# Performance work log

Measured on AMD Instinct MI355X. Metric: run time of the kernel, lower is better.

Reference implementation:

```python
import jax, jax.numpy as jnp
import numpy as np

D_MODEL = 1024
N_HEAD = 16
D_K = D_MODEL // N_HEAD


def setup_inputs() -> dict:
    key = jax.random.key(0)
    ks = jax.random.split(key, 11)
    B, S = 2, 2048
    scale = 1.0 / np.sqrt(D_MODEL)
    inp = {
        "q": jax.random.normal(ks[0], (B, S, D_MODEL), jnp.float32),
        "k": jax.random.normal(ks[1], (B, S, D_MODEL), jnp.float32),
        "v": jax.random.normal(ks[2], (B, S, D_MODEL), jnp.float32),
        "Wq": jax.random.normal(ks[3], (D_MODEL, D_MODEL), jnp.float32) * scale,
        "bq": jnp.zeros((D_MODEL,), jnp.float32),
        "Wk": jax.random.normal(ks[4], (D_MODEL, D_MODEL), jnp.float32) * scale,
        "bk": jnp.zeros((D_MODEL,), jnp.float32),
        "Wv": jax.random.normal(ks[5], (D_MODEL, D_MODEL), jnp.float32) * scale,
        "bv": jnp.zeros((D_MODEL,), jnp.float32),
        "Wo": jax.random.normal(ks[6], (D_MODEL, D_MODEL), jnp.float32) * scale,
        "bo": jnp.zeros((D_MODEL,), jnp.float32),
    }
    return inp


def reference(q, k, v, Wq, bq, Wk, bk, Wv, bv, Wo, bo):
    B, S, _ = q.shape
    # QKV projections, split heads: [B, H, S, d_k]
    def proj(x, W, b):
        y = x @ W + b  # [B, S, D]
        return y.reshape(B, -1, N_HEAD, D_K).transpose(0, 2, 1, 3)

    qh = proj(q, Wq, bq)
    kh = proj(k, Wk, bk)
    vh = proj(v, Wv, bv)

    # sigmoid attention (no row normalization)
    scores = jnp.einsum("bhsd,bhtd->bhst", qh, kh) / jnp.sqrt(jnp.float32(D_K))
    attn = jax.nn.sigmoid(scores)  # [B, H, S, S]
    ctx = jnp.einsum("bhst,bhtd->bhsd", attn, vh)

    # merge heads and output projection
    ctx = ctx.transpose(0, 2, 1, 3).reshape(B, S, D_MODEL)
    return ctx @ Wo + bo
```

## Files before the change

kernel.cpp:

```cpp
#include <hip/hip_runtime.h>
#include <stdint.h>

typedef _Float16 f16;
typedef _Float16 f16x4 __attribute__((ext_vector_type(4)));
typedef _Float16 f16x8 __attribute__((ext_vector_type(8)));
typedef float f32x4 __attribute__((ext_vector_type(4)));

#define D_MODEL 1024
#define N_HEAD 16
#define BATCH 2
#define SEQ 2048
#define MTOT 4096
#define NQKV 3072

__device__ __forceinline__ void llds16(const void* g, void* l) {
  __builtin_amdgcn_global_load_lds(
      (const __attribute__((address_space(1))) unsigned int*)g,
      (__attribute__((address_space(3))) unsigned int*)l, 16, 0, 0);
}

__device__ __forceinline__ float fast_rcp(float x) {
#if __has_builtin(__builtin_amdgcn_rcpf)
  return __builtin_amdgcn_rcpf(x);
#else
  return 1.0f / x;
#endif
}

__global__ void k_cvt(const float* __restrict__ src, f16* __restrict__ dst, int n) {
  int i = (blockIdx.x * blockDim.x + threadIdx.x) * 4;
  if (i < n) {
    const float4 v = *(const float4*)(src + i);
    f16x4 o;
    o.x = (f16)v.x; o.y = (f16)v.y; o.z = (f16)v.z; o.w = (f16)v.w;
    *(f16x4*)(dst + i) = o;
  }
}

__global__ void k_tw(const float* __restrict__ Wq, const float* __restrict__ Wk,
                     const float* __restrict__ Wv, const float* __restrict__ Wo,
                     f16* __restrict__ WqkvT, f16* __restrict__ WoT) {
  __shared__ float t[32][33];
  const int z = blockIdx.z;
  const float* W = (z == 0) ? Wq : (z == 1) ? Wk : (z == 2) ? Wv : Wo;
  f16* dst = (z < 3) ? (WqkvT + (size_t)z * 1024 * 1024) : WoT;
  const int bx = blockIdx.x * 32, by = blockIdx.y * 32;
  const int tx = threadIdx.x, ty = threadIdx.y;
#pragma unroll
  for (int i = 0; i < 32; i += 8)
    t[ty + i][tx] = W[(size_t)(by + ty + i) * 1024 + bx + tx];
  __syncthreads();
#pragma unroll
  for (int i = 0; i < 32; i += 8)
    dst[(size_t)(bx + ty + i) * 1024 + by + tx] = (f16)t[tx][ty + i];
}

template <int Nd, bool OUTF32>
__global__ __launch_bounds__(512, 4) void k_gemm(const f16* __restrict__ A0,
                                                 const f16* __restrict__ A1,
                                                 const f16* __restrict__ A2,
                                                 const f16* __restrict__ BT,
                                                 const float* __restrict__ b0,
                                                 const float* __restrict__ b1,
                                                 const float* __restrict__ b2,
                                                 void* __restrict__ Cout) {
  constexpr int Kd = 1024;
  constexpr int NBX = Nd / 128;
  constexpr int NWG = (MTOT / 128) * NBX;
  __shared__ __align__(16) f16 As[2][8192];
  __shared__ __align__(16) f16 Bs[2][8192];
  int id = blockIdx.x;
  id = (id & 7) * (NWG / 8) + (id >> 3);
  const int n0 = (id % NBX) * 128, m0 = (id / NBX) * 128;
  const f16* A = (Nd == 1024) ? A0 : (n0 < 1024 ? A0 : n0 < 2048 ? A1 : A2);
  const int tid = threadIdx.x, w = tid >> 6, ln = tid & 63;
  const int wm = w >> 2, wn = w & 3;
  f32x4 acc[4][2] = {};

  auto stage = [&](int buf, int kt) {
    const int k0 = kt * 64;
#pragma unroll
    for (int i = 0; i < 2; ++i) {
      const int c = w * 2 + i;
      const int r = c * 8 + (ln >> 3);
      const int g = ln & 7;
      const int ko = k0 + ((g ^ (r & 7)) * 8);
      llds16(A + (size_t)(m0 + r) * Kd + ko, &As[buf][c * 512]);
      llds16(BT + (size_t)(n0 + r) * Kd + ko, &Bs[buf][c * 512]);
    }
  };
  stage(0, 0);
  __syncthreads();
  int cur = 0;
  for (int kt = 0; kt < Kd / 64; ++kt) {
    if (kt < Kd / 64 - 1) stage(cur ^ 1, kt + 1);
#pragma unroll
    for (int kk = 0; kk < 2; ++kk) {
      f16x8 af[4], bf[2];
#pragma unroll
      for (int mi = 0; mi < 4; ++mi) {
        const int r = wm * 64 + mi * 16 + (ln & 15);
        const int g = kk * 4 + (ln >> 4);
        af[mi] = *(const f16x8*)(&As[cur][r * 64 + ((g ^ (r & 7)) * 8)]);
      }
#pragma unroll
      for (int nf = 0; nf < 2; ++nf) {
        const int r = wn * 32 + nf * 16 + (ln & 15);
        const int g = kk * 4 + (ln >> 4);
        bf[nf] = *(const f16x8*)(&Bs[cur][r * 64 + ((g ^ (r & 7)) * 8)]);
      }
#pragma unroll
      for (int mi = 0; mi < 4; ++mi)
#pragma unroll
        for (int nf = 0; nf < 2; ++nf)
          acc[mi][nf] = __builtin_amdgcn_mfma_f32_16x16x32_f16(af[mi], bf[nf], acc[mi][nf], 0, 0, 0);
    }
    __syncthreads();
    cur ^= 1;
  }
  const float* bb = (Nd == 1024) ? b0 : (n0 < 1024 ? b0 : n0 < 2048 ? b1 : b2);
  const int nb = n0 & 1023;
#pragma unroll
  for (int mi = 0; mi < 4; ++mi)
#pragma unroll
    for (int nf = 0; nf < 2; ++nf)
#pragma unroll
      for (int r = 0; r < 4; ++r) {
        const int row = m0 + wm * 64 + mi * 16 + (ln >> 4) * 4 + r;
        const int cl = wn * 32 + nf * 16 + (ln & 15);
        const float val = acc[mi][nf][r] + bb[nb + cl];
        if (OUTF32)
          ((float*)Cout)[(size_t)row * Nd + n0 + cl] = val;
        else
          ((f16*)Cout)[(size_t)row * Nd + n0 + cl] = (f16)val;
      }
}

__global__ void k_tv(const f16* __restrict__ QKV, f16* __restrict__ Vt) {
  const int sb = blockIdx.x, h = blockIdx.y, b = blockIdx.z;
  const int t = threadIdx.x;
  const int d = t & 63, si = (t >> 6) * 16;
  const int s0 = sb * 64 + si;
  const f16* src = QKV + ((size_t)b * SEQ + s0) * NQKV + 2048 + h * 64 + d;
  f16x8 v0, v1;
#pragma unroll
  for (int j = 0; j < 8; ++j) v0[j] = src[(size_t)j * NQKV];
#pragma unroll
  for (int j = 0; j < 8; ++j) v1[j] = src[(size_t)(j + 8) * NQKV];
  f16* dst = Vt + ((size_t)(b * N_HEAD + h) * 64 + d) * SEQ + s0;
  *(f16x8*)dst = v0;
  *(f16x8*)(dst + 8) = v1;
}

__global__ __launch_bounds__(256, 4) void k_attn(const f16* __restrict__ QKV,
                                                 const f16* __restrict__ Vt,
                                                 f16* __restrict__ ctx) {
  __shared__ __align__(16) f16 Ks[2][4096];
  __shared__ __align__(16) f16 Vs[2][4096];
  __shared__ __align__(16) f16 Pl[4][1024];
  int id = blockIdx.x;
  id = (id & 7) * 128 + (id >> 3);
  const int qt = id & 31, h = (id >> 5) & 15, b = id >> 9;
  const int tid = threadIdx.x, w = tid >> 6, ln = tid & 63;
  const int s0 = qt * 64;
  const f16* Qb = QKV + ((size_t)b * SEQ) * NQKV + h * 64;
  const f16* Kb = QKV + ((size_t)b * SEQ) * NQKV + 1024 + h * 64;
  const f16* Vtb = Vt + (size_t)(b * N_HEAD + h) * 64 * SEQ;
  const int q = ln & 15;
  f16x8 aq[2];
  {
    const int qrow = s0 + w * 16 + q;
#pragma unroll
    for (int kk = 0; kk < 2; ++kk)
      aq[kk] = *(const f16x8*)(Qb + (size_t)qrow * NQKV + kk * 32 + (ln >> 4) * 8);
  }
  f32x4 oacc[4] = {};
  auto stage = [&](int buf, int kt) {
    const int kv0 = kt * 64;
#pragma unroll
    for (int i = 0; i < 2; ++i) {
      const int c = w * 2 + i;
      const int r = c * 8 + (ln >> 3);
      const int g = ln & 7;
      llds16(Kb + (size_t)(kv0 + r) * NQKV + ((g ^ (r & 7)) * 8), &Ks[buf][c * 512]);
      llds16(Vtb + (size_t)r * SEQ + kv0 + ((g ^ (r & 7)) * 8), &Vs[buf][c * 512]);
    }
  };
  stage(0, 0);
  __syncthreads();
  int cur = 0;
  for (int kt = 0; kt < SEQ / 64; ++kt) {
    if (kt < SEQ / 64 - 1) stage(cur ^ 1, kt + 1);
    f32x4 sacc[4] = {};
#pragma unroll
    for (int kk = 0; kk < 2; ++kk) {
      f16x8 ak[4];
#pragma unroll
      for (int nt = 0; nt < 4; ++nt) {
        const int kv = nt * 16 + (ln & 15);
        const int g = kk * 4 + (ln >> 4);
        ak[nt] = *(const f16x8*)(&Ks[cur][kv * 64 + ((g ^ (kv & 7)) * 8)]);
      }
#pragma unroll
      for (int nt = 0; nt < 4; ++nt)
        sacc[nt] = __builtin_amdgcn_mfma_f32_16x16x32_f16(ak[nt], aq[kk], sacc[nt], 0, 0, 0);
    }
#pragma unroll
    for (int nt = 0; nt < 4; ++nt) {
      f16x4 pk;
#pragma unroll
      for (int r = 0; r < 4; ++r) {
        const float e = __expf(sacc[nt][r] * -0.125f);
        pk[r] = (f16)fast_rcp(1.0f + e);
      }
      const int gw = nt * 4 + (ln >> 4);
      *(f16x4*)(&Pl[w][q * 64 + ((gw ^ (2 * (q & 7))) * 4)]) = pk;
    }
#pragma unroll
    for (int kk = 0; kk < 2; ++kk) {
      const int gr = kk * 8 + (ln >> 4) * 2;
      const f16x8 ap = *(const f16x8*)(&Pl[w][q * 64 + ((gr ^ (2 * (q & 7))) * 4)]);
      f16x8 bv[4];
#pragma unroll
      for (int nt = 0; nt < 4; ++nt) {
        const int d = nt * 16 + (ln & 15);
        const int g = kk * 4 + (ln >> 4);
        bv[nt] = *(const f16x8*)(&Vs[cur][d * 64 + ((g ^ (d & 7)) * 8)]);
      }
#pragma unroll
      for (int nt = 0; nt < 4; ++nt)
        oacc[nt] = __builtin_amdgcn_mfma_f32_16x16x32_f16(ap, bv[nt], oacc[nt], 0, 0, 0);
    }
    __syncthreads();
    cur ^= 1;
  }
  f16* cb = ctx + ((size_t)b * SEQ + s0 + w * 16) * D_MODEL + h * 64;
#pragma unroll
  for (int nt = 0; nt < 4; ++nt)
#pragma unroll
    for (int r = 0; r < 4; ++r)
      cb[((ln >> 4) * 4 + r) * D_MODEL + nt * 16 + (ln & 15)] = (f16)oacc[nt][r];
}

extern "C" void kernel_launch(void* const* d_in, const int* in_sizes, int n_in,
                              void* d_out, int out_size, void* d_ws, size_t ws_size,
                              hipStream_t stream) {
  (void)in_sizes; (void)n_in; (void)out_size; (void)ws_size;
  const float* q  = (const float*)d_in[0];
  const float* k  = (const float*)d_in[1];
  const float* v  = (const float*)d_in[2];
  const float* Wq = (const float*)d_in[3];
  const float* bq = (const float*)d_in[4];
  const float* Wk = (const float*)d_in[5];
  const float* bk = (const float*)d_in[6];
  const float* Wv = (const float*)d_in[7];
  const float* bv = (const float*)d_in[8];
  const float* Wo = (const float*)d_in[9];
  const float* bo = (const float*)d_in[10];
  float* out = (float*)d_out;

  char* p = (char*)d_ws;
  const size_t SZ_X = (size_t)MTOT * D_MODEL * sizeof(f16);
  f16* qb    = (f16*)p; p += SZ_X;
  f16* kb    = (f16*)p; p += SZ_X;
  f16* vb    = (f16*)p; p += SZ_X;
  f16* WqkvT = (f16*)p; p += 3 * (size_t)1024 * 1024 * sizeof(f16);
  f16* WoT   = (f16*)p; p += (size_t)1024 * 1024 * sizeof(f16);
  f16* QKVb  = (f16*)p; p += (size_t)MTOT * NQKV * sizeof(f16);
  f16* Vtb   = (f16*)p; p += SZ_X;
  f16* ctx   = (f16*)p; p += SZ_X;

  const int n = MTOT * D_MODEL;
  k_cvt<<<n / 4 / 256, 256, 0, stream>>>(q, qb, n);
  k_cvt<<<n / 4 / 256, 256, 0, stream>>>(k, kb, n);
  k_cvt<<<n / 4 / 256, 256, 0, stream>>>(v, vb, n);
  k_tw<<<dim3(32, 32, 4), dim3(32, 8), 0, stream>>>(Wq, Wk, Wv, Wo, WqkvT, WoT);
  k_gemm<NQKV, false><<<(MTOT / 128) * (NQKV / 128), 512, 0, stream>>>(
      qb, kb, vb, WqkvT, bq, bk, bv, QKVb);
  k_tv<<<dim3(SEQ / 64, N_HEAD, BATCH), 256, 0, stream>>>(QKVb, Vtb);
  k_attn<<<SEQ / 64 * N_HEAD * BATCH, 256, 0, stream>>>(QKVb, Vtb, ctx);
  k_gemm<1024, true><<<(MTOT / 128) * (1024 / 128), 512, 0, stream>>>(
      ctx, ctx, ctx, WoT, bo, bo, bo, out);
}
```

Baseline: 245.5 us.

## Use 32x32 MFMA attention with register P, fuse V transpose and merge casts

The attention kernel switches to 32x32x16 MFMA tiles with 128-query blocks. It keeps the sigmoid probabilities in registers via permlane32 swaps instead of round-tripping through LDS. The V transpose kernel is removed: the QKV GEMM epilogue writes V directly in transposed layout, and the three f32->f16 conversion launches are merged into one. This reduces launches, LDS traffic and extra memory passes, at the cost of fewer attention workgroups (512), lower declared occupancy, and scattered f16x4 stores in the GEMM epilogue.

Result: faster. 233.9 us (-4.7%).

```diff
diff --git a/kernel.cpp b/kernel.cpp
--- a/kernel.cpp
+++ b/kernel.cpp
@@ -5,6 +5,8 @@
 typedef _Float16 f16x4 __attribute__((ext_vector_type(4)));
 typedef _Float16 f16x8 __attribute__((ext_vector_type(8)));
 typedef float f32x4 __attribute__((ext_vector_type(4)));
+typedef float f32x16 __attribute__((ext_vector_type(16)));
+typedef unsigned int u32;
 
 #define D_MODEL 1024
 #define N_HEAD 16
@@ -27,14 +29,25 @@
 #endif
 }
 
-__global__ void k_cvt(const float* __restrict__ src, f16* __restrict__ dst, int n) {
-  int i = (blockIdx.x * blockDim.x + threadIdx.x) * 4;
-  if (i < n) {
-    const float4 v = *(const float4*)(src + i);
-    f16x4 o;
-    o.x = (f16)v.x; o.y = (f16)v.y; o.z = (f16)v.z; o.w = (f16)v.w;
-    *(f16x4*)(dst + i) = o;
-  }
+#define SIG(x) fast_rcp(1.0f + __expf((x) * -0.125f))
+
+__device__ __forceinline__ u32 pk2(float a, float b) {
+  auto h = __builtin_amdgcn_cvt_pkrtz(a, b);
+  return __builtin_bit_cast(u32, h);
+}
+
+__global__ void k_cvt3(const float* __restrict__ q, const float* __restrict__ k,
+                       const float* __restrict__ v, f16* __restrict__ dst) {
+  const int idx = (blockIdx.x * 256 + threadIdx.x) * 8;
+  const int seg = idx >> 22;
+  const int off = idx & ((1 << 22) - 1);
+  const float* s = (seg == 0) ? q : (seg == 1) ? k : v;
+  const float4 a = *(const float4*)(s + off);
+  const float4 b = *(const float4*)(s + off + 4);
+  f16x8 o;
+  o[0] = (f16)a.x; o[1] = (f16)a.y; o[2] = (f16)a.z; o[3] = (f16)a.w;
+  o[4] = (f16)b.x; o[5] = (f16)b.y; o[6] = (f16)b.z; o[7] = (f16)b.w;
+  *(f16x8*)(dst + idx) = o;
 }
 
 __global__ void k_tw(const float* __restrict__ Wq, const float* __restrict__ Wk,
@@ -55,7 +68,7 @@
     dst[(size_t)(bx + ty + i) * 1024 + by + tx] = (f16)t[tx][ty + i];
 }
 
-template <int Nd, bool OUTF32>
+template <int Nd, int MODE>
 __global__ __launch_bounds__(512, 4) void k_gemm(const f16* __restrict__ A0,
                                                  const f16* __restrict__ A1,
                                                  const f16* __restrict__ A2,
@@ -63,7 +76,8 @@
                                                  const float* __restrict__ b0,
                                                  const float* __restrict__ b1,
                                                  const float* __restrict__ b2,
-                                                 void* __restrict__ Cout) {
+                                                 void* __restrict__ Cout,
+                                                 f16* __restrict__ Vt) {
   constexpr int Kd = 1024;
   constexpr int NBX = Nd / 128;
   constexpr int NWG = (MTOT / 128) * NBX;
@@ -120,61 +134,62 @@
   }
   const float* bb = (Nd == 1024) ? b0 : (n0 < 1024 ? b0 : n0 < 2048 ? b1 : b2);
   const int nb = n0 & 1023;
-#pragma unroll
-  for (int mi = 0; mi < 4; ++mi)
-#pragma unroll
-    for (int nf = 0; nf < 2; ++nf)
-#pragma unroll
-      for (int r = 0; r < 4; ++r) {
-        const int row = m0 + wm * 64 + mi * 16 + (ln >> 4) * 4 + r;
+  if (MODE == 0 && n0 >= 2048) {
+#pragma unroll
+    for (int mi = 0; mi < 4; ++mi)
+#pragma unroll
+      for (int nf = 0; nf < 2; ++nf) {
         const int cl = wn * 32 + nf * 16 + (ln & 15);
-        const float val = acc[mi][nf][r] + bb[nb + cl];
-        if (OUTF32)
-          ((float*)Cout)[(size_t)row * Nd + n0 + cl] = val;
-        else
-          ((f16*)Cout)[(size_t)row * Nd + n0 + cl] = (f16)val;
-      }
-}
-
-__global__ void k_tv(const f16* __restrict__ QKV, f16* __restrict__ Vt) {
-  const int sb = blockIdx.x, h = blockIdx.y, b = blockIdx.z;
-  const int t = threadIdx.x;
-  const int d = t & 63, si = (t >> 6) * 16;
-  const int s0 = sb * 64 + si;
-  const f16* src = QKV + ((size_t)b * SEQ + s0) * NQKV + 2048 + h * 64 + d;
-  f16x8 v0, v1;
-#pragma unroll
-  for (int j = 0; j < 8; ++j) v0[j] = src[(size_t)j * NQKV];
-#pragma unroll
-  for (int j = 0; j < 8; ++j) v1[j] = src[(size_t)(j + 8) * NQKV];
-  f16* dst = Vt + ((size_t)(b * N_HEAD + h) * 64 + d) * SEQ + s0;
-  *(f16x8*)dst = v0;
-  *(f16x8*)(dst + 8) = v1;
-}
-
-__global__ __launch_bounds__(256, 4) void k_attn(const f16* __restrict__ QKV,
+        const int colg = n0 - 2048 + cl;
+        const int hd = colg >> 6, d = colg & 63;
+        const int row0 = m0 + wm * 64 + mi * 16 + (ln >> 4) * 4;
+        const int bI = row0 >> 11, s = row0 & 2047;
+        const float bias = bb[nb + cl];
+        f16x4 pv;
+#pragma unroll
+        for (int r = 0; r < 4; ++r) pv[r] = (f16)(acc[mi][nf][r] + bias);
+        *(f16x4*)(&Vt[((size_t)(bI * 16 + hd) * 64 + d) * SEQ + s]) = pv;
+      }
+  } else {
+#pragma unroll
+    for (int mi = 0; mi < 4; ++mi)
+#pragma unroll
+      for (int nf = 0; nf < 2; ++nf)
+#pragma unroll
+        for (int r = 0; r < 4; ++r) {
+          const int row = m0 + wm * 64 + mi * 16 + (ln >> 4) * 4 + r;
+          const int cl = wn * 32 + nf * 16 + (ln & 15);
+          const float val = acc[mi][nf][r] + bb[nb + cl];
+          if (MODE == 1)
+            ((float*)Cout)[(size_t)row * Nd + n0 + cl] = val;
+          else
+            ((f16*)Cout)[(size_t)row * Nd + n0 + cl] = (f16)val;
+        }
+  }
+}
+
+__global__ __launch_bounds__(256, 2) void k_attn(const f16* __restrict__ QKV,
                                                  const f16* __restrict__ Vt,
                                                  f16* __restrict__ ctx) {
   __shared__ __align__(16) f16 Ks[2][4096];
   __shared__ __align__(16) f16 Vs[2][4096];
-  __shared__ __align__(16) f16 Pl[4][1024];
   int id = blockIdx.x;
-  id = (id & 7) * 128 + (id >> 3);
-  const int qt = id & 31, h = (id >> 5) & 15, b = id >> 9;
+  id = (id & 7) * 64 + (id >> 3);
+  const int qt = id & 15, hd = (id >> 4) & 15, b = id >> 8;
   const int tid = threadIdx.x, w = tid >> 6, ln = tid & 63;
-  const int s0 = qt * 64;
-  const f16* Qb = QKV + ((size_t)b * SEQ) * NQKV + h * 64;
-  const f16* Kb = QKV + ((size_t)b * SEQ) * NQKV + 1024 + h * 64;
-  const f16* Vtb = Vt + (size_t)(b * N_HEAD + h) * 64 * SEQ;
-  const int q = ln & 15;
-  f16x8 aq[2];
-  {
-    const int qrow = s0 + w * 16 + q;
-#pragma unroll
-    for (int kk = 0; kk < 2; ++kk)
-      aq[kk] = *(const f16x8*)(Qb + (size_t)qrow * NQKV + kk * 32 + (ln >> 4) * 8);
-  }
-  f32x4 oacc[4] = {};
+  const int lh = ln >> 5, l31 = ln & 31;
+  const int q0 = qt * 128 + w * 32;
+  const f16* Qb = QKV + ((size_t)b * SEQ) * NQKV + hd * 64;
+  const f16* Kb = QKV + ((size_t)b * SEQ) * NQKV + 1024 + hd * 64;
+  const f16* Vtb = Vt + (size_t)(b * N_HEAD + hd) * 64 * SEQ;
+
+  f16x8 aq[4];
+#pragma unroll
+  for (int kk = 0; kk < 4; ++kk)
+    aq[kk] = *(const f16x8*)(Qb + (size_t)(q0 + l31) * NQKV + kk * 16 + lh * 8);
+
+  f32x16 oacc0 = {}, oacc1 = {};
+
   auto stage = [&](int buf, int kt) {
     const int kv0 = kt * 64;
 #pragma unroll
@@ -191,55 +206,64 @@
   int cur = 0;
   for (int kt = 0; kt < SEQ / 64; ++kt) {
     if (kt < SEQ / 64 - 1) stage(cur ^ 1, kt + 1);
-    f32x4 sacc[4] = {};
-#pragma unroll
-    for (int kk = 0; kk < 2; ++kk) {
-      f16x8 ak[4];
-#pragma unroll
-      for (int nt = 0; nt < 4; ++nt) {
-        const int kv = nt * 16 + (ln & 15);
-        const int g = kk * 4 + (ln >> 4);
-        ak[nt] = *(const f16x8*)(&Ks[cur][kv * 64 + ((g ^ (kv & 7)) * 8)]);
-      }
-#pragma unroll
-      for (int nt = 0; nt < 4; ++nt)
-        sacc[nt] = __builtin_amdgcn_mfma_f32_16x16x32_f16(ak[nt], aq[kk], sacc[nt], 0, 0, 0);
-    }
-#pragma unroll
-    for (int nt = 0; nt < 4; ++nt) {
-      f16x4 pk;
-#pragma unroll
-      for (int r = 0; r < 4; ++r) {
-        const float e = __expf(sacc[nt][r] * -0.125f);
-        pk[r] = (f16)fast_rcp(1.0f + e);
-      }
-      const int gw = nt * 4 + (ln >> 4);
-      *(f16x4*)(&Pl[w][q * 64 + ((gw ^ (2 * (q & 7))) * 4)]) = pk;
-    }
-#pragma unroll
-    for (int kk = 0; kk < 2; ++kk) {
-      const int gr = kk * 8 + (ln >> 4) * 2;
-      const f16x8 ap = *(const f16x8*)(&Pl[w][q * 64 + ((gr ^ (2 * (q & 7))) * 4)]);
-      f16x8 bv[4];
-#pragma unroll
-      for (int nt = 0; nt < 4; ++nt) {
-        const int d = nt * 16 + (ln & 15);
-        const int g = kk * 4 + (ln >> 4);
-        bv[nt] = *(const f16x8*)(&Vs[cur][d * 64 + ((g ^ (d & 7)) * 8)]);
-      }
-#pragma unroll
-      for (int nt = 0; nt < 4; ++nt)
-        oacc[nt] = __builtin_amdgcn_mfma_f32_16x16x32_f16(ap, bv[nt], oacc[nt], 0, 0, 0);
+    f32x16 sacc0 = {}, sacc1 = {};
+#pragma unroll
+    for (int kk = 0; kk < 4; ++kk) {
+      {
+        const int r = l31;
+        const f16x8 ak = *(const f16x8*)(&Ks[cur][r * 64 + (((kk * 2 + lh) ^ (r & 7)) * 8)]);
+        sacc0 = __builtin_amdgcn_mfma_f32_32x32x16_f16(ak, aq[kk], sacc0, 0, 0, 0);
+      }
+      {
+        const int r = 32 + l31;
+        const f16x8 ak = *(const f16x8*)(&Ks[cur][r * 64 + (((kk * 2 + lh) ^ (r & 7)) * 8)]);
+        sacc1 = __builtin_amdgcn_mfma_f32_32x32x16_f16(ak, aq[kk], sacc1, 0, 0, 0);
+      }
+    }
+    f16x8 pa[4];
+#pragma unroll
+    for (int kvt = 0; kvt < 2; ++kvt) {
+      const f32x16 sc = kvt ? sacc1 : sacc0;
+#pragma unroll
+      for (int hf = 0; hf < 2; ++hf) {
+        const int b8 = hf * 8;
+        u32 X = pk2(SIG(sc[b8 + 0]), SIG(sc[b8 + 1]));
+        u32 Y = pk2(SIG(sc[b8 + 2]), SIG(sc[b8 + 3]));
+        u32 Z = pk2(SIG(sc[b8 + 4]), SIG(sc[b8 + 5]));
+        u32 W = pk2(SIG(sc[b8 + 6]), SIG(sc[b8 + 7]));
+        asm volatile("v_permlane32_swap_b32 %0, %1" : "+v"(X), "+v"(Z));
+        asm volatile("v_permlane32_swap_b32 %0, %1" : "+v"(Y), "+v"(W));
+        union { u32 uw[4]; f16x8 v; } u;
+        u.uw[0] = X; u.uw[1] = Y; u.uw[2] = Z; u.uw[3] = W;
+        pa[kvt * 2 + hf] = u.v;
+      }
+    }
+#pragma unroll
+    for (int c = 0; c < 4; ++c) {
+      {
+        const int d = l31;
+        const f16x8 bv = *(const f16x8*)(&Vs[cur][d * 64 + (((c * 2 + lh) ^ (d & 7)) * 8)]);
+        oacc0 = __builtin_amdgcn_mfma_f32_32x32x16_f16(pa[c], bv, oacc0, 0, 0, 0);
+      }
+      {
+        const int d = 32 + l31;
+        const f16x8 bv = *(const f16x8*)(&Vs[cur][d * 64 + (((c * 2 + lh) ^ (d & 7)) * 8)]);
+        oacc1 = __builtin_amdgcn_mfma_f32_32x32x16_f16(pa[c], bv, oacc1, 0, 0, 0);
+      }
     }
     __syncthreads();
     cur ^= 1;
   }
-  f16* cb = ctx + ((size_t)b * SEQ + s0 + w * 16) * D_MODEL + h * 64;
-#pragma unroll
-  for (int nt = 0; nt < 4; ++nt)
-#pragma unroll
-    for (int r = 0; r < 4; ++r)
-      cb[((ln >> 4) * 4 + r) * D_MODEL + nt * 16 + (ln & 15)] = (f16)oacc[nt][r];
+#pragma unroll
+  for (int dt = 0; dt < 2; ++dt) {
+    const int dcol = hd * 64 + dt * 32 + l31;
+#pragma unroll
+    for (int r = 0; r < 16; ++r) {
+      const int ql = (r & 3) + 8 * (r >> 2) + 4 * lh;
+      const float v = dt ? oacc1[r] : oacc0[r];
+      ctx[((size_t)b * SEQ + q0 + ql) * D_MODEL + dcol] = (f16)v;
+    }
+  }
 }
 
 extern "C" void kernel_launch(void* const* d_in, const int* in_sizes, int n_in,
@@ -261,24 +285,20 @@
 
   char* p = (char*)d_ws;
   const size_t SZ_X = (size_t)MTOT * D_MODEL * sizeof(f16);
-  f16* qb    = (f16*)p; p += SZ_X;
-  f16* kb    = (f16*)p; p += SZ_X;
-  f16* vb    = (f16*)p; p += SZ_X;
+  f16* qb    = (f16*)p; p += 3 * SZ_X;
   f16* WqkvT = (f16*)p; p += 3 * (size_t)1024 * 1024 * sizeof(f16);
   f16* WoT   = (f16*)p; p += (size_t)1024 * 1024 * sizeof(f16);
   f16* QKVb  = (f16*)p; p += (size_t)MTOT * NQKV * sizeof(f16);
   f16* Vtb   = (f16*)p; p += SZ_X;
   f16* ctx   = (f16*)p; p += SZ_X;
-
-  const int n = MTOT * D_MODEL;
-  k_cvt<<<n / 4 / 256, 256, 0, stream>>>(q, qb, n);
-  k_cvt<<<n / 4 / 256, 256, 0, stream>>>(k, kb, n);
-  k_cvt<<<n / 4 / 256, 256, 0, stream>>>(v, vb, n);
+  f16* kb = qb + (size_t)MTOT * D_MODEL;
+  f16* vb = kb + (size_t)MTOT * D_MODEL;
+
+  k_cvt3<<<3 * MTOT * D_MODEL / 2048, 256, 0, stream>>>(q, k, v, qb);
   k_tw<<<dim3(32, 32, 4), dim3(32, 8), 0, stream>>>(Wq, Wk, Wv, Wo, WqkvT, WoT);
-  k_gemm<NQKV, false><<<(MTOT / 128) * (NQKV / 128), 512, 0, stream>>>(
-      qb, kb, vb, WqkvT, bq, bk, bv, QKVb);
-  k_tv<<<dim3(SEQ / 64, N_HEAD, BATCH), 256, 0, stream>>>(QKVb, Vtb);
-  k_attn<<<SEQ / 64 * N_HEAD * BATCH, 256, 0, stream>>>(QKVb, Vtb, ctx);
-  k_gemm<1024, true><<<(MTOT / 128) * (1024 / 128), 512, 0, stream>>>(
-      ctx, ctx, ctx, WoT, bo, bo, bo, out);
-}
+  k_gemm<NQKV, 0><<<(MTOT / 128) * (NQKV / 128), 512, 0, stream>>>(
+      qb, kb, vb, WqkvT, bq, bk, bv, QKVb, Vtb);
+  k_attn<<<(SEQ / 128) * N_HEAD * BATCH, 256, 0, stream>>>(QKVb, Vtb, ctx);
+  k_gemm<1024, 1><<<(MTOT / 128) * (1024 / 128), 512, 0, stream>>>(
+      ctx, ctx, ctx, WoT, bo, bo, bo, out, nullptr);
+}
```
